# Kernel optimization log

Hardware: AMD Instinct MI355X
Metric: run time of the kernel (lower is better)

Reference implementation:

```python
import jax, jax.numpy as jnp
import numpy as np

B, N, D = 4, 2048, 768
H, HD = 12, 64  # heads, head_dim; D == H*HD
SCALE = HD ** -0.5


def setup_inputs() -> dict:
    key = jax.random.key(0)
    k1, k2, k3 = jax.random.split(key, 3)
    x = jax.random.normal(k1, (B, N, D), dtype=jnp.float32)
    w_qkv = jax.random.normal(k2, (D, 3 * D), dtype=jnp.float32) * (D ** -0.5)
    b_qkv = jnp.zeros((3 * D,), dtype=jnp.float32)
    w_proj = jax.random.normal(k3, (D, D), dtype=jnp.float32) * (D ** -0.5)
    b_proj = jnp.zeros((D,), dtype=jnp.float32)
    return {"x": x, "w_qkv": w_qkv, "b_qkv": b_qkv, "w_proj": w_proj, "b_proj": b_proj}


def reference(x, w_qkv, b_qkv, w_proj, b_proj):
    # 1. QKV projection, split into 3
    qkv = x @ w_qkv + b_qkv                      # (B, N, 3D)
    q, k, v = jnp.split(qkv, 3, axis=-1)         # each (B, N, D)
    # 2. reshape to (B, H, N, HD)
    def to_heads(t):
        return t.reshape(B, N, H, HD).transpose(0, 2, 1, 3)
    q, k, v = to_heads(q), to_heads(k), to_heads(v)
    # 3-4. scaled dot-product attention (full score matrix, as in the original)
    scores = jnp.einsum("bhnd,bhmd->bhnm", q, k) * SCALE   # (B, H, N, N)
    attn = jax.nn.softmax(scores, axis=-1)
    # 5. dropout p=0.0 -> identity (eval)
    # 6. weighted sum
    out = jnp.einsum("bhnm,bhmd->bhnd", attn, v)           # (B, H, N, HD)
    # 7. merge heads
    out = out.transpose(0, 2, 1, 3).reshape(B, N, D)
    # 8. output projection
    return out @ w_proj + b_proj
```

## Files before the change

### kernel.cpp

```cpp
#include <hip/hip_runtime.h>
#include <stdint.h>
#include <stddef.h>


typedef __bf16 bf16x8 __attribute__((ext_vector_type(8)));
typedef float  f32x4  __attribute__((ext_vector_type(4)));
typedef float  f32x16 __attribute__((ext_vector_type(16)));
typedef unsigned int u32x2 __attribute__((ext_vector_type(2)));

__device__ __forceinline__ float bf2f(unsigned short u){
  union { unsigned int i; float f; } x; x.i = ((unsigned int)u) << 16; return x.f;
}
__device__ __forceinline__ unsigned short fast2bf(float f){
  union { float f; unsigned int i; } x; x.f = f;
  return (unsigned short)((x.i + 0x8000u) >> 16);
}
__device__ __forceinline__ unsigned int fbits(float f){
  union { float f; unsigned int i; } x; x.f = f; return x.i;
}
__device__ __forceinline__ unsigned int cvtpk_bf16(float lo, float hi){
  unsigned int r;
  asm("v_cvt_pk_bf16_f32 %0, %1, %2" : "=v"(r) : "v"(lo), "v"(hi));
  return r;
}
__device__ __forceinline__ void plswap32(unsigned int &a, unsigned int &b){
#if __has_builtin(__builtin_amdgcn_permlane32_swap)
  u32x2 r = __builtin_amdgcn_permlane32_swap(a, b, false, false);
  a = r.x; b = r.y;
#else
  asm volatile("v_permlane32_swap_b32 %0, %1" : "+v"(a), "+v"(b));
#endif
}

#if __has_builtin(__builtin_amdgcn_exp2f)
  #define EXP2F(x) __builtin_amdgcn_exp2f(x)
#else
  #define EXP2F(x) exp2f(x)
#endif

#define GLD16(gp, lp) __builtin_amdgcn_global_load_lds( \
  (__attribute__((address_space(1))) void*)(uintptr_t)(gp), \
  (__attribute__((address_space(3))) void*)(unsigned int)(uintptr_t)(lp), 16, 0, 0)

__global__ void f32_to_bf16(const float* __restrict__ in,
                            unsigned short* __restrict__ out, int n){
  int i = (blockIdx.x * 256 + threadIdx.x) * 4;
  if(i < n){
    float4 v = *(const float4*)(in + i);
    ushort4 o;
    o.x = fast2bf(v.x); o.y = fast2bf(v.y); o.z = fast2bf(v.z); o.w = fast2bf(v.w);
    *(ushort4*)(out + i) = o;
  }
}

__global__ void transpose_f32_bf16(const float* __restrict__ W,
                                   unsigned short* __restrict__ Wt, int K, int N){
  __shared__ float tile[32][33];
  int n0 = blockIdx.x * 32, k0 = blockIdx.y * 32;
  int tx = threadIdx.x, ty = threadIdx.y;
  for(int i = ty; i < 32; i += 8) tile[i][tx] = W[(size_t)(k0 + i) * N + (n0 + tx)];
  __syncthreads();
  for(int i = ty; i < 32; i += 8) Wt[(size_t)(n0 + i) * K + (k0 + tx)] = fast2bf(tile[tx][i]);
}

__global__ __launch_bounds__(256) void transpose_v(const unsigned short* __restrict__ qkv,
                                                   unsigned short* __restrict__ VT){
  __shared__ __align__(16) unsigned short Ts[64*72];
  const int t  = threadIdx.x;
  const int jt = blockIdx.x;
  const int bh = blockIdx.y;
  const int b = bh / 12, h = bh - b*12;
  const unsigned short* src = qkv + (size_t)(b*2048 + jt*64)*2304 + 1536 + h*64;
  #pragma unroll
  for(int c = t; c < 512; c += 256){
    int j = c >> 3, d0 = (c & 7) * 8;
    *(uint4*)&Ts[j*72 + d0] = *(const uint4*)(src + (size_t)j*2304 + d0);
  }
  __syncthreads();
  unsigned short* dst = VT + (size_t)bh*64*2048 + jt*64;
  #pragma unroll
  for(int c = t; c < 512; c += 256){
    int d = c >> 3, j0 = (c & 7) * 8;
    ushort4 lo, hi;
    lo.x = Ts[(j0+0)*72 + d]; lo.y = Ts[(j0+1)*72 + d];
    lo.z = Ts[(j0+2)*72 + d]; lo.w = Ts[(j0+3)*72 + d];
    hi.x = Ts[(j0+4)*72 + d]; hi.y = Ts[(j0+5)*72 + d];
    hi.z = Ts[(j0+6)*72 + d]; hi.w = Ts[(j0+7)*72 + d];
    *(ushort4*)(dst + (size_t)d*2048 + j0)     = lo;
    *(ushort4*)(dst + (size_t)d*2048 + j0 + 4) = hi;
  }
}

template<typename OT>
__global__ __launch_bounds__(256) void gemm_bt(const unsigned short* __restrict__ A,
                                               const unsigned short* __restrict__ Bt,
                                               const float* __restrict__ bias,
                                               OT* __restrict__ C,
                                               int M, int N, int K, int lda){
  __shared__ __align__(16) unsigned short As[2][128*32];
  __shared__ __align__(16) unsigned short Bs[2][128*32];
  const int tid  = threadIdx.x;
  const int lane = tid & 63, w = tid >> 6;
  const int m0 = blockIdx.y * 128, n0 = blockIdx.x * 128;

  f32x4 acc[4][4];
  #pragma unroll
  for(int i=0;i<4;i++)
    #pragma unroll
    for(int j=0;j<4;j++) acc[i][j] = (f32x4){0.f,0.f,0.f,0.f};

  const int c0 = w*64 + lane, c1 = c0 + 256;
  const unsigned short* Ag0 = A  + (size_t)(m0 + (c0>>2)) * lda + (c0&3)*8;
  const unsigned short* Ag1 = A  + (size_t)(m0 + (c1>>2)) * lda + (c1&3)*8;
  const unsigned short* Bg0 = Bt + (size_t)(n0 + (c0>>2)) * K   + (c0&3)*8;
  const unsigned short* Bg1 = Bt + (size_t)(n0 + (c1>>2)) * K   + (c1&3)*8;

  const int wm = w & 1, wn = w >> 1;
  const int quad = lane >> 4, l15 = lane & 15;

  GLD16(Ag0, As[0] +        w*512);
  GLD16(Ag1, As[0] + 2048 + w*512);
  GLD16(Bg0, Bs[0] +        w*512);
  GLD16(Bg1, Bs[0] + 2048 + w*512);

  int cur = 0;
  for(int kt = 0; kt < K; kt += 32){
    __syncthreads();
    if(kt + 32 < K){
      int nx = cur ^ 1;
      GLD16(Ag0 + kt + 32, As[nx] +        w*512);
      GLD16(Ag1 + kt + 32, As[nx] + 2048 + w*512);
      GLD16(Bg0 + kt + 32, Bs[nx] +        w*512);
      GLD16(Bg1 + kt + 32, Bs[nx] + 2048 + w*512);
    }

    bf16x8 af[4], bfr[4];
    #pragma unroll
    for(int mt=0;mt<4;mt++) af[mt]  = *(const bf16x8*)&As[cur][(wm*64 + mt*16 + l15)*32 + quad*8];
    #pragma unroll
    for(int nt=0;nt<4;nt++) bfr[nt] = *(const bf16x8*)&Bs[cur][(wn*64 + nt*16 + l15)*32 + quad*8];
    #pragma unroll
    for(int mt=0;mt<4;mt++)
      #pragma unroll
      for(int nt=0;nt<4;nt++)
        acc[mt][nt] = __builtin_amdgcn_mfma_f32_16x16x32_bf16(af[mt], bfr[nt], acc[mt][nt], 0, 0, 0);
    cur ^= 1;
  }

  #pragma unroll
  for(int nt=0;nt<4;nt++){
    int col = n0 + wn*64 + nt*16 + l15;
    float bv = bias[col];
    #pragma unroll
    for(int mt=0;mt<4;mt++){
      int row0 = m0 + wm*64 + mt*16 + quad*4;
      #pragma unroll
      for(int i=0;i<4;i++){
        float v = acc[mt][nt][i] + bv;
        if constexpr (sizeof(OT) == 2)
          C[(size_t)(row0 + i) * N + col] = (OT)fast2bf(v);
        else
          C[(size_t)(row0 + i) * N + col] = (OT)v;
      }
    }
  }
}

__global__ __launch_bounds__(256, 3) void attn_mfma(unsigned short* __restrict__ qkv,
                                                    const unsigned short* __restrict__ VT){
  __shared__ __align__(16) unsigned short Ks[2][4096];
  __shared__ __align__(16) unsigned short Vs[2][4096];
  __shared__ float linv_lds[4*32];

  const int t    = threadIdx.x;
  const int lane = t & 63, w = t >> 6;
  const int l31  = lane & 31, hi = lane >> 5;

  const int bid = blockIdx.x;
  const int wg  = (bid & 7) * 96 + (bid >> 3);
  const int b   = wg / 192;
  const int rem = wg - b * 192;
  const int h   = rem >> 4;
  const int bx  = rem & 15;
  const int q0  = bx * 128 + w * 32;

  unsigned short* Qg = qkv + (size_t)(b*2048 + q0)*2304 + h*64;

  const float QSCALE = 0.125f * 1.4426950408889634f;
  bf16x8 qf[4];
  #pragma unroll
  for(int c=0;c<4;c++){
    uint4 raw = *(const uint4*)(Qg + (size_t)l31*2304 + c*16 + hi*8);
    const unsigned short* rp = (const unsigned short*)&raw;
    unsigned short o[8];
    #pragma unroll
    for(int e=0;e<8;e++) o[e] = fast2bf(bf2f(rp[e]) * QSCALE);
    qf[c] = *(const bf16x8*)o;
  }

  f32x16 oacc0, oacc1;
  #pragma unroll
  for(int i=0;i<16;i++){ oacc0[i] = 0.f; oacc1[i] = 0.f; }
  float lp0=0.f, lp1=0.f, lp2=0.f, lp3=0.f;

  const int gA = w*2, gB = w*2 + 1;
  const unsigned short* gK = qkv + (size_t)(b*2048)*2304 + 768 + h*64;
  const unsigned short* gV = VT + (size_t)(b*12 + h)*64*2048;
  const size_t kOffA = (size_t)((gA>>2)*32 + l31)*2304 + (gA&3)*16 + hi*8;
  const size_t kOffB = (size_t)((gB>>2)*32 + l31)*2304 + (gB&3)*16 + hi*8;
  const size_t vOffA = (size_t)((gA&1)*32 + l31)*2048 + (gA>>2)*32 + ((gA>>1)&1)*16 + hi*8;
  const size_t vOffB = (size_t)((gB&1)*32 + l31)*2048 + (gB>>2)*32 + ((gB>>1)&1)*16 + hi*8;

  GLD16(gK + kOffA, Ks[0] + gA*512);
  GLD16(gK + kOffB, Ks[0] + gB*512);
  GLD16(gV + vOffA, Vs[0] + gA*512);
  GLD16(gV + vOffB, Vs[0] + gB*512);

  int cur = 0;
  #pragma unroll 1
  for(int it = 0; it < 32; ++it){
    __syncthreads();
    if(it + 1 < 32){
      int nx = cur ^ 1;
      gK += (size_t)64*2304;
      gV += 64;
      GLD16(gK + kOffA, Ks[nx] + gA*512);
      GLD16(gK + kOffB, Ks[nx] + gB*512);
      GLD16(gV + vOffA, Vs[nx] + gA*512);
      GLD16(gV + vOffB, Vs[nx] + gB*512);
    }
    const unsigned short* Kst = Ks[cur] + lane*8;
    const unsigned short* Vst = Vs[cur] + lane*8;

    #pragma unroll
    for(int ks = 0; ks < 2; ++ks){
      bf16x8 kf0 = *(const bf16x8*)(Kst + (ks*4 + 0)*512);
      bf16x8 kf1 = *(const bf16x8*)(Kst + (ks*4 + 1)*512);
      bf16x8 kf2 = *(const bf16x8*)(Kst + (ks*4 + 2)*512);
      bf16x8 kf3 = *(const bf16x8*)(Kst + (ks*4 + 3)*512);

      f32x16 sacc;
      #pragma unroll
      for(int i=0;i<16;i++) sacc[i] = 0.f;
      __builtin_amdgcn_s_setprio(1);
      sacc = __builtin_amdgcn_mfma_f32_32x32x16_bf16(kf0, qf[0], sacc, 0, 0, 0);
      sacc = __builtin_amdgcn_mfma_f32_32x32x16_bf16(kf1, qf[1], sacc, 0, 0, 0);
      sacc = __builtin_amdgcn_mfma_f32_32x32x16_bf16(kf2, qf[2], sacc, 0, 0, 0);
      sacc = __builtin_amdgcn_mfma_f32_32x32x16_bf16(kf3, qf[3], sacc, 0, 0, 0);
      __builtin_amdgcn_s_setprio(0);

      bf16x8 vf00 = *(const bf16x8*)(Vst + (ks*4 + 0)*512);
      bf16x8 vf01 = *(const bf16x8*)(Vst + (ks*4 + 1)*512);
      bf16x8 vf10 = *(const bf16x8*)(Vst + (ks*4 + 2)*512);
      bf16x8 vf11 = *(const bf16x8*)(Vst + (ks*4 + 3)*512);

      float p[16];
      #pragma unroll
      for(int r=0;r<16;r++) p[r] = EXP2F(sacc[r]);
      #pragma unroll
      for(int r=0;r<16;r+=4){
        lp0 += p[r]; lp1 += p[r+1]; lp2 += p[r+2]; lp3 += p[r+3];
      }

      unsigned int d0 = cvtpk_bf16(p[0],  p[1]);
      unsigned int d1 = cvtpk_bf16(p[2],  p[3]);
      unsigned int d2 = cvtpk_bf16(p[4],  p[5]);
      unsigned int d3 = cvtpk_bf16(p[6],  p[7]);
      unsigned int d4 = cvtpk_bf16(p[8],  p[9]);
      unsigned int d5 = cvtpk_bf16(p[10], p[11]);
      unsigned int d6 = cvtpk_bf16(p[12], p[13]);
      unsigned int d7 = cvtpk_bf16(p[14], p[15]);
      plswap32(d0, d2); plswap32(d1, d3);
      plswap32(d4, d6); plswap32(d5, d7);
      unsigned int c0w[4] = {d0, d1, d2, d3};
      unsigned int c1w[4] = {d4, d5, d6, d7};
      bf16x8 pa0 = *(const bf16x8*)c0w;
      bf16x8 pa1 = *(const bf16x8*)c1w;

      __builtin_amdgcn_s_setprio(1);
      oacc0 = __builtin_amdgcn_mfma_f32_32x32x16_bf16(pa0, vf00, oacc0, 0, 0, 0);
      oacc1 = __builtin_amdgcn_mfma_f32_32x32x16_bf16(pa0, vf01, oacc1, 0, 0, 0);
      oacc0 = __builtin_amdgcn_mfma_f32_32x32x16_bf16(pa1, vf10, oacc0, 0, 0, 0);
      oacc1 = __builtin_amdgcn_mfma_f32_32x32x16_bf16(pa1, vf11, oacc1, 0, 0, 0);
      __builtin_amdgcn_s_setprio(0);
    }
    cur ^= 1;
  }

  float lpart = (lp0 + lp1) + (lp2 + lp3);
  lpart += __shfl_xor(lpart, 32, 64);
  if(lane < 32) linv_lds[w*32 + l31] = 1.0f / lpart;
  __syncthreads();

  #pragma unroll
  for(int r=0;r<16;r++){
    int qrow = (r&3) + 8*(r>>2) + 4*hi;
    float li = linv_lds[w*32 + qrow];
    unsigned short* row = Qg + (size_t)qrow*2304;
    row[l31]      = fast2bf(oacc0[r] * li);
    row[32 + l31] = fast2bf(oacc1[r] * li);
  }
}

extern "C" void kernel_launch(void* const* d_in, const int* in_sizes, int n_in,
                              void* d_out, int out_size, void* d_ws, size_t ws_size,
                              hipStream_t stream){
  const float* x      = (const float*)d_in[0];
  const float* w_qkv  = (const float*)d_in[1];
  const float* b_qkv  = (const float*)d_in[2];
  const float* w_proj = (const float*)d_in[3];
  const float* b_proj = (const float*)d_in[4];
  float* out = (float*)d_out;

  unsigned short* xb      = (unsigned short*)d_ws;
  unsigned short* Wt_qkv  = xb      + (size_t)8192*768;
  unsigned short* Wt_proj = Wt_qkv  + (size_t)2304*768;
  unsigned short* qkvb    = Wt_proj + (size_t)768*768;
  unsigned short* VT      = xb;

  f32_to_bf16<<<(8192*768)/1024, 256, 0, stream>>>(x, xb, 8192*768);
  transpose_f32_bf16<<<dim3(72, 24), dim3(32, 8), 0, stream>>>(w_qkv,  Wt_qkv,  768, 2304);
  transpose_f32_bf16<<<dim3(24, 24), dim3(32, 8), 0, stream>>>(w_proj, Wt_proj, 768, 768);

  gemm_bt<unsigned short><<<dim3(2304/128, 8192/128), 256, 0, stream>>>(
      xb, Wt_qkv, b_qkv, qkvb, 8192, 2304, 768, 768);

  transpose_v<<<dim3(32, 48), 256, 0, stream>>>(qkvb, VT);

  attn_mfma<<<768, 256, 0, stream>>>(qkvb, VT);

  gemm_bt<float><<<dim3(768/128, 8192/128), 256, 0, stream>>>(
      qkvb, Wt_proj, b_proj, out, 8192, 768, 768, 2304);
}
```

Baseline: 220.6 us.

## Stage K/V through registers with coalesced row loads and XOR-swizzled LDS

Replaces the direct global-to-LDS loads (GLD16) for K and V tiles with coalesced 16-byte global loads into registers. These registers are written into a single combined, XOR-swizzled LDS buffer after the compute of the current tile, which software-pipelines the prefetch across the MFMA work. Fragment reads use a matching swizzled address pattern to avoid bank conflicts. It also drops the s_setprio hints around the MFMA groups. This costs extra VGPRs for the in-flight tiles and adds explicit LDS stores, which may pressure the 3-wave occupancy target.

New measurement: 220.9 us. Within noise of the previous version (+0.1%).

```diff
diff --git a/kernel.cpp b/kernel.cpp
--- a/kernel.cpp
+++ b/kernel.cpp
@@ -14,9 +14,6 @@
 __device__ __forceinline__ unsigned short fast2bf(float f){
   union { float f; unsigned int i; } x; x.f = f;
   return (unsigned short)((x.i + 0x8000u) >> 16);
-}
-__device__ __forceinline__ unsigned int fbits(float f){
-  union { float f; unsigned int i; } x; x.f = f; return x.i;
 }
 __device__ __forceinline__ unsigned int cvtpk_bf16(float lo, float hi){
   unsigned int r;
@@ -168,8 +165,7 @@
 
 __global__ __launch_bounds__(256, 3) void attn_mfma(unsigned short* __restrict__ qkv,
                                                     const unsigned short* __restrict__ VT){
-  __shared__ __align__(16) unsigned short Ks[2][4096];
-  __shared__ __align__(16) unsigned short Vs[2][4096];
+  __shared__ __align__(16) unsigned short KV[2][8192];
   __shared__ float linv_lds[4*32];
 
   const int t    = threadIdx.x;
@@ -203,56 +199,70 @@
   for(int i=0;i<16;i++){ oacc0[i] = 0.f; oacc1[i] = 0.f; }
   float lp0=0.f, lp1=0.f, lp2=0.f, lp3=0.f;
 
-  const int gA = w*2, gB = w*2 + 1;
-  const unsigned short* gK = qkv + (size_t)(b*2048)*2304 + 768 + h*64;
-  const unsigned short* gV = VT + (size_t)(b*12 + h)*64*2048;
-  const size_t kOffA = (size_t)((gA>>2)*32 + l31)*2304 + (gA&3)*16 + hi*8;
-  const size_t kOffB = (size_t)((gB>>2)*32 + l31)*2304 + (gB&3)*16 + hi*8;
-  const size_t vOffA = (size_t)((gA&1)*32 + l31)*2048 + (gA>>2)*32 + ((gA>>1)&1)*16 + hi*8;
-  const size_t vOffB = (size_t)((gB&1)*32 + l31)*2048 + (gB>>2)*32 + ((gB>>1)&1)*16 + hi*8;
-
-  GLD16(gK + kOffA, Ks[0] + gA*512);
-  GLD16(gK + kOffB, Ks[0] + gB*512);
-  GLD16(gV + vOffA, Vs[0] + gA*512);
-  GLD16(gV + vOffB, Vs[0] + gB*512);
+  const int r8 = lane >> 3, c8 = lane & 7;
+  const unsigned short* gK = qkv + (size_t)(b*2048)*2304 + 768 + h*64
+                           + (size_t)(w*8 + r8)*2304 + c8*8;
+  const unsigned short* gV = VT + (size_t)(b*12 + h)*64*2048
+                           + (size_t)(w*8 + r8)*2048 + c8*8;
+
+  int kwoff[2], vwoff[2];
+  #pragma unroll
+  for(int L=0; L<2; ++L){
+    int sl = w*8 + r8 + 32*(c8&1);
+    kwoff[L] = (L*4 + (c8>>1))*1024 + ((sl ^ (c8 ^ (L<<1))) * 16);
+    int gVg  = (c8>>2)*4 + ((c8>>1)&1)*2 + L;
+    int pV   = ((((gVg&3)<<1) | (c8&1)) ^ ((gVg>>2)<<1));
+    vwoff[L] = 8192 + gVg*1024 + ((sl ^ pV) * 16);
+  }
+
+  const int lin2 = (lane*16) ^ (hi*16);
+  const int EG[8] = {0, 32, 64, 96, 32, 0, 96, 64};
+
+  uint4 ka0 = *(const uint4*)(gK);
+  uint4 ka1 = *(const uint4*)(gK + (size_t)32*2304);
+  uint4 va0 = *(const uint4*)(gV);
+  uint4 va1 = *(const uint4*)(gV + (size_t)32*2048);
+  {
+    char* W0 = (char*)KV[0];
+    *(uint4*)(W0 + kwoff[0]) = ka0;
+    *(uint4*)(W0 + kwoff[1]) = ka1;
+    *(uint4*)(W0 + vwoff[0]) = va0;
+    *(uint4*)(W0 + vwoff[1]) = va1;
+  }
 
   int cur = 0;
   #pragma unroll 1
   for(int it = 0; it < 32; ++it){
     __syncthreads();
     if(it + 1 < 32){
-      int nx = cur ^ 1;
       gK += (size_t)64*2304;
       gV += 64;
-      GLD16(gK + kOffA, Ks[nx] + gA*512);
-      GLD16(gK + kOffB, Ks[nx] + gB*512);
-      GLD16(gV + vOffA, Vs[nx] + gA*512);
-      GLD16(gV + vOffB, Vs[nx] + gB*512);
-    }
-    const unsigned short* Kst = Ks[cur] + lane*8;
-    const unsigned short* Vst = Vs[cur] + lane*8;
+      ka0 = *(const uint4*)(gK);
+      ka1 = *(const uint4*)(gK + (size_t)32*2304);
+      va0 = *(const uint4*)(gV);
+      va1 = *(const uint4*)(gV + (size_t)32*2048);
+    }
+    const char* Kc = (const char*)KV[cur];
 
     #pragma unroll
     for(int ks = 0; ks < 2; ++ks){
-      bf16x8 kf0 = *(const bf16x8*)(Kst + (ks*4 + 0)*512);
-      bf16x8 kf1 = *(const bf16x8*)(Kst + (ks*4 + 1)*512);
-      bf16x8 kf2 = *(const bf16x8*)(Kst + (ks*4 + 2)*512);
-      bf16x8 kf3 = *(const bf16x8*)(Kst + (ks*4 + 3)*512);
+      bf16x8 kf0 = *(const bf16x8*)(Kc + (ks*4 + 0)*1024 + (lin2 ^ EG[ks*4 + 0]));
+      bf16x8 kf1 = *(const bf16x8*)(Kc + (ks*4 + 1)*1024 + (lin2 ^ EG[ks*4 + 1]));
+      bf16x8 kf2 = *(const bf16x8*)(Kc + (ks*4 + 2)*1024 + (lin2 ^ EG[ks*4 + 2]));
+      bf16x8 kf3 = *(const bf16x8*)(Kc + (ks*4 + 3)*1024 + (lin2 ^ EG[ks*4 + 3]));
 
       f32x16 sacc;
       #pragma unroll
       for(int i=0;i<16;i++) sacc[i] = 0.f;
-      __builtin_amdgcn_s_setprio(1);
       sacc = __builtin_amdgcn_mfma_f32_32x32x16_bf16(kf0, qf[0], sacc, 0, 0, 0);
       sacc = __builtin_amdgcn_mfma_f32_32x32x16_bf16(kf1, qf[1], sacc, 0, 0, 0);
       sacc = __builtin_amdgcn_mfma_f32_32x32x16_bf16(kf2, qf[2], sacc, 0, 0, 0);
       sacc = __builtin_amdgcn_mfma_f32_32x32x16_bf16(kf3, qf[3], sacc, 0, 0, 0);
-      __builtin_amdgcn_s_setprio(0);
-
-      bf16x8 vf00 = *(const bf16x8*)(Vst + (ks*4 + 0)*512);
-      bf16x8 vf01 = *(const bf16x8*)(Vst + (ks*4 + 1)*512);
-      bf16x8 vf10 = *(const bf16x8*)(Vst + (ks*4 + 2)*512);
-      bf16x8 vf11 = *(const bf16x8*)(Vst + (ks*4 + 3)*512);
+
+      bf16x8 vf00 = *(const bf16x8*)(Kc + 8192 + (ks*4 + 0)*1024 + (lin2 ^ EG[ks*4 + 0]));
+      bf16x8 vf01 = *(const bf16x8*)(Kc + 8192 + (ks*4 + 1)*1024 + (lin2 ^ EG[ks*4 + 1]));
+      bf16x8 vf10 = *(const bf16x8*)(Kc + 8192 + (ks*4 + 2)*1024 + (lin2 ^ EG[ks*4 + 2]));
+      bf16x8 vf11 = *(const bf16x8*)(Kc + 8192 + (ks*4 + 3)*1024 + (lin2 ^ EG[ks*4 + 3]));
 
       float p[16];
       #pragma unroll
@@ -277,12 +287,18 @@
       bf16x8 pa0 = *(const bf16x8*)c0w;
       bf16x8 pa1 = *(const bf16x8*)c1w;
 
-      __builtin_amdgcn_s_setprio(1);
       oacc0 = __builtin_amdgcn_mfma_f32_32x32x16_bf16(pa0, vf00, oacc0, 0, 0, 0);
       oacc1 = __builtin_amdgcn_mfma_f32_32x32x16_bf16(pa0, vf01, oacc1, 0, 0, 0);
       oacc0 = __builtin_amdgcn_mfma_f32_32x32x16_bf16(pa1, vf10, oacc0, 0, 0, 0);
       oacc1 = __builtin_amdgcn_mfma_f32_32x32x16_bf16(pa1, vf11, oacc1, 0, 0, 0);
-      __builtin_amdgcn_s_setprio(0);
+    }
+
+    if(it + 1 < 32){
+      char* Wn = (char*)KV[cur ^ 1];
+      *(uint4*)(Wn + kwoff[0]) = ka0;
+      *(uint4*)(Wn + kwoff[1]) = ka1;
+      *(uint4*)(Wn + vwoff[0]) = va0;
+      *(uint4*)(Wn + vwoff[1]) = va1;
     }
     cur ^= 1;
   }
```
